# Kernel tuning notes

Hardware: AMD Instinct MI355X
Metric: run time of the kernel (lower is better)

Reference implementation:

```python
import jax, jax.numpy as jnp
import numpy as np

NL_IN = 0.5      # init kwarg nl_in
CONS = 1e-10     # epsilon added to rates
POISSON_GAIN = 20.0

def setup_inputs() -> dict:
    key = jax.random.key(0)
    k1, k2 = jax.random.split(key)
    shape = (8, 4, 28, 256, 256)  # (bs, c, s, h, w)
    spec_data = jax.random.uniform(k1, shape, dtype=jnp.float32)
    filt = jax.random.uniform(k2, shape, dtype=jnp.float32)
    return {"spec_data": spec_data, "filter": filt}

def reference(spec_data, filter):
    # cap_data = sum over (channel, spectral) dims -> [bs, h, w], then [bs, h, w, 1]
    cap = jnp.sum(spec_data * filter, axis=(1, 2))[..., None]

    # noise synthesis (need_noise=True path)
    poisson_t = jnp.full_like(cap, POISSON_GAIN * NL_IN)
    dark_t = jnp.full_like(cap, 1.0 * NL_IN)
    gauss_t = jnp.full_like(cap, 1.0 * NL_IN)
    peak = cap + CONS

    key = jax.random.key(1)
    kp, kd, kg = jax.random.split(key, 3)
    pnoisy = jax.random.poisson(kp, peak).astype(cap.dtype)
    dnoisy = jax.random.poisson(kd, dark_t).astype(cap.dtype)
    gnoisy = jax.random.normal(kg, cap.shape, dtype=cap.dtype) * gauss_t

    noisy = (pnoisy + dnoisy + gnoisy) * poisson_t / 255.0
    return (noisy, peak, dark_t, gauss_t ** 2)
```

## Files before the change

kernel.cpp:

```cpp
#include <hip/hip_runtime.h>
#include <cstdint>
#include <cstddef>

#pragma clang fp contract(off)

#define N_PIX    524288
#define CSPLANES 112
#define PLANE    65536
#define DCH      48
#define NBLK     256

struct TF2 { uint32_t a, b; };

__host__ __device__ constexpr uint32_t rotl32(uint32_t x, int d) {
  return (x << d) | (x >> (32 - d));
}

__host__ __device__ constexpr TF2 threefry(uint32_t k0, uint32_t k1,
                                           uint32_t c0, uint32_t c1) {
  uint32_t ks2 = k0 ^ k1 ^ 0x1BD11BDAu;
  uint32_t x0 = c0 + k0;
  uint32_t x1 = c1 + k1;
  const int R0[4] = {13, 15, 26, 6};
  const int R1[4] = {17, 29, 16, 24};
  for (int i = 0; i < 4; ++i) { x0 += x1; x1 = rotl32(x1, R0[i]); x1 ^= x0; }
  x0 += k1;  x1 += ks2 + 1u;
  for (int i = 0; i < 4; ++i) { x0 += x1; x1 = rotl32(x1, R1[i]); x1 ^= x0; }
  x0 += ks2; x1 += k0 + 2u;
  for (int i = 0; i < 4; ++i) { x0 += x1; x1 = rotl32(x1, R0[i]); x1 ^= x0; }
  x0 += k0;  x1 += k1 + 3u;
  for (int i = 0; i < 4; ++i) { x0 += x1; x1 = rotl32(x1, R1[i]); x1 ^= x0; }
  x0 += k1;  x1 += ks2 + 4u;
  for (int i = 0; i < 4; ++i) { x0 += x1; x1 = rotl32(x1, R0[i]); x1 ^= x0; }
  x0 += ks2; x1 += k0 + 5u;
  return TF2{x0, x1};
}

struct Chains {
  uint32_t kg0, kg1;
  uint32_t rj0a[DCH], rj0b[DCH], rj1a[DCH], rj1b[DCH];
  uint32_t kda[DCH], kdb[DCH];
  uint32_t kpa[DCH], kpb[DCH];
};

__host__ __device__ constexpr Chains make_chains() {
  Chains c{};
  TF2 kp = threefry(0u, 1u, 0u, 0u);
  TF2 kd = threefry(0u, 1u, 0u, 1u);
  TF2 kg = threefry(0u, 1u, 0u, 2u);
  c.kg0 = kg.a; c.kg1 = kg.b;
  {
    uint32_t a = kp.a, b = kp.b;
    for (int i = 0; i < DCH; ++i) {
      TF2 nk = threefry(a, b, 0u, 0u);
      TF2 s0 = threefry(a, b, 0u, 1u);
      TF2 s1 = threefry(a, b, 0u, 2u);
      c.rj0a[i] = s0.a; c.rj0b[i] = s0.b;
      c.rj1a[i] = s1.a; c.rj1b[i] = s1.b;
      a = nk.a; b = nk.b;
    }
  }
  {
    uint32_t a = kd.a, b = kd.b;
    for (int i = 0; i < DCH; ++i) {
      TF2 nk = threefry(a, b, 0u, 0u);
      TF2 sk = threefry(a, b, 0u, 1u);
      c.kda[i] = sk.a; c.kdb[i] = sk.b;
      a = nk.a; b = nk.b;
    }
  }
  {
    uint32_t a = kp.a, b = kp.b;
    for (int i = 0; i < DCH; ++i) {
      TF2 nk = threefry(a, b, 0u, 0u);
      TF2 sk = threefry(a, b, 0u, 1u);
      c.kpa[i] = sk.a; c.kpb[i] = sk.b;
      a = nk.a; b = nk.b;
    }
  }
  return c;
}

__constant__ Chains G = make_chains();

__device__ inline float u01(uint32_t k0, uint32_t k1, uint32_t j) {
  TF2 r = threefry(k0, k1, 0u, j);
  uint32_t bits = r.a ^ r.b;
  return __uint_as_float((bits >> 9) | 0x3F800000u) - 1.0f;
}

__device__ inline float xla_lgamma(float x_in) {
  float z = x_in - 1.0f;
  float x = 1.0f;
  x = x + 676.520368121885098567009190444019f    / ((z + 0.0f) + 1.0f);
  x = x + (-1259.13921672240287047156078755283f) / ((z + 1.0f) + 1.0f);
  x = x + 771.3234287776530788486528258894f      / ((z + 2.0f) + 1.0f);
  x = x + (-176.61502916214059906584551354f)     / ((z + 3.0f) + 1.0f);
  x = x + 12.507343278686904814458936853f        / ((z + 4.0f) + 1.0f);
  x = x + (-0.13857109526572011689554707f)       / ((z + 5.0f) + 1.0f);
  x = x + 9.984369578019570859563e-6f            / ((z + 6.0f) + 1.0f);
  x = x + 1.50563273514931155834e-7f             / ((z + 7.0f) + 1.0f);
  float t = 7.5f + z;
  float log_t = 2.0149030205422647f + log1pf(z / 7.5f);
  return 0.91893853320467274178f + ((z + 0.5f) - t / log_t) * log_t + logf(x);
}

__device__ inline float xla_erfinv(float xx) {
  float w = -log1pf(-(xx * xx));
  float p;
  if (w < 5.0f) {
    float ww = w - 2.5f;
    p = 2.81022636e-08f;
    p = 3.43273939e-07f + p * ww;
    p = -3.5233877e-06f + p * ww;
    p = -4.39150654e-06f + p * ww;
    p = 0.00021858087f + p * ww;
    p = -0.00125372503f + p * ww;
    p = -0.00417768164f + p * ww;
    p = 0.246640727f + p * ww;
    p = 1.50140941f + p * ww;
  } else {
    float ww = sqrtf(w) - 3.0f;
    p = -0.000200214257f;
    p = 0.000100950558f + p * ww;
    p = 0.00134934322f + p * ww;
    p = -0.00367342844f + p * ww;
    p = 0.00573950773f + p * ww;
    p = -0.0076224613f + p * ww;
    p = 0.00943887047f + p * ww;
    p = 1.00167406f + p * ww;
    p = 2.83297682f + p * ww;
  }
  return p * xx;
}

__device__ inline float xla_normal(uint32_t j) {
  const float lo = -0.999999940395355224609375f;
  float f = u01(G.kg0, G.kg1, j);
  float u = f * (1.0f - lo) + lo;
  u = fmaxf(lo, u);
  return 1.41421356237309504880f * xla_erfinv(u);
}

__device__ inline int knuth_sample(const uint32_t* ka, const uint32_t* kb,
                                   uint32_t j, float lam) {
  const float neg = -lam;
  int k = 0;
  float lp = 0.0f;
  #pragma unroll 1
  for (int i = 0; i < DCH; ++i) {
    if (!(lp > neg)) break;
    ++k;
    float uu = u01(ka[i], kb[i], j);
    lp = lp + logf(uu);
  }
  return k - 1;
}

struct RejC { float lam, loglam, a, b, inva, vr; };

__device__ inline RejC make_rc(float lam) {
  RejC rc;
  rc.lam = lam;
  rc.loglam = logf(lam);
  rc.b = 0.931f + 2.53f * sqrtf(lam);
  rc.a = -0.059f + 0.02483f * rc.b;
  rc.inva = 1.1239f + 1.1328f / (rc.b - 3.4f);
  rc.vr = 0.9277f - 3.6224f / (rc.b - 2.0f);
  return rc;
}

__device__ inline bool rej_step(const RejC& rc, uint32_t j, int i, float* kout) {
  float u = u01(G.rj0a[i], G.rj0b[i], j) - 0.5f;
  float v = u01(G.rj1a[i], G.rj1b[i], j);
  float us = 0.5f - fabsf(u);
  float k = floorf(((2.0f * rc.a / us + rc.b) * u + rc.lam) + 0.43f);
  *kout = k;
  bool accept1 = (us >= 0.07f) && (v <= rc.vr);
  if (accept1) return true;
  bool reject = (k < 0.0f) || ((us < 0.013f) && (v > us));
  if (reject) return false;
  float s = logf(v * rc.inva / (rc.a / (us * us) + rc.b));
  float t = (-rc.lam + k * rc.loglam) - xla_lgamma(k + 1.0f);
  return s <= t;
}

__device__ inline unsigned first_accept(const RejC& rc, uint32_t j) {
  unsigned F = DCH;
  #pragma unroll 1
  for (int i = 0; i < DCH; ++i) {
    float kc;
    if (rej_step(rc, j, i, &kc)) { F = (unsigned)(i + 1); break; }
  }
  return F;
}

__device__ inline float resolve_pix(const RejC& rc, float peak, uint32_t j, int T) {
  if (peak >= 10.0f) {
    float kk = -1.0f;
    #pragma unroll 1
    for (int i = T - 1; i >= 0; --i) {
      float kc;
      if (rej_step(rc, j, i, &kc)) { kk = kc; break; }
    }
    return (float)(int)kk;
  } else if (peak <= 0.0f) {
    return 0.0f;
  } else {
    return (float)knuth_sample(G.kpa, G.kpb, j, peak);
  }
}

__global__ __launch_bounds__(1024) void fused_kernel(const float* __restrict__ spec,
                                                     const float* __restrict__ filt,
                                                     float* __restrict__ out,
                                                     unsigned* __restrict__ sync) {
  const int tid = threadIdx.x;
  const int pixbase = blockIdx.x << 11;
  const int b_img = pixbase >> 16;
  const int hw = (pixbase & 65535) + (tid << 1);
  const size_t base = (size_t)b_img * ((size_t)CSPLANES * PLANE) + (size_t)hw;
  const float* sp = spec + base;
  const float* fp = filt + base;

  float a0 = 0.f, a1 = 0.f;
  #pragma unroll 8
  for (int cs = 0; cs < CSPLANES; ++cs) {
    const float2 s = *reinterpret_cast<const float2*>(sp + (size_t)cs * PLANE);
    const float2 f = *reinterpret_cast<const float2*>(fp + (size_t)cs * PLANE);
    a0 += s.x * f.x;
    a1 += s.y * f.y;
  }

  const uint32_t j0 = (uint32_t)(pixbase + (tid << 1));
  const uint32_t j1 = j0 + 1u;
  const float pk0 = a0 + 1e-10f;
  const float pk1 = a1 + 1e-10f;
  const float d0 = (float)knuth_sample(G.kda, G.kdb, j0, 0.5f);
  const float d1 = (float)knuth_sample(G.kda, G.kdb, j1, 0.5f);
  const float g0 = xla_normal(j0) * 0.5f;
  const float g1 = xla_normal(j1) * 0.5f;
  const RejC rc0 = make_rc(pk0);
  const RejC rc1 = make_rc(pk1);
  unsigned F0 = first_accept(rc0, j0);
  unsigned F1 = first_accept(rc1, j1);
  unsigned F = F0 > F1 ? F0 : F1;

  for (int off = 32; off; off >>= 1) {
    unsigned o = (unsigned)__shfl_down((int)F, off, 64);
    F = F > o ? F : o;
  }
  __shared__ unsigned sred[16];
  __shared__ int sT;
  if ((tid & 63) == 0) sred[tid >> 6] = F;
  __syncthreads();
  if (tid == 0) {
    unsigned m = sred[0];
    #pragma unroll
    for (int i = 1; i < 16; ++i) m = m > sred[i] ? m : sred[i];
    __hip_atomic_fetch_max(&sync[0], m, __ATOMIC_RELAXED, __HIP_MEMORY_SCOPE_AGENT);
    __hip_atomic_fetch_add(&sync[1], 1u, __ATOMIC_ACQ_REL, __HIP_MEMORY_SCOPE_AGENT);
    while (__hip_atomic_load(&sync[1], __ATOMIC_ACQUIRE, __HIP_MEMORY_SCOPE_AGENT) < (unsigned)NBLK) {
      __builtin_amdgcn_s_sleep(8);
    }
    sT = (int)__hip_atomic_load(&sync[0], __ATOMIC_RELAXED, __HIP_MEMORY_SCOPE_AGENT);
  }
  __syncthreads();
  const int T = sT;

  const float pv0 = resolve_pix(rc0, pk0, j0, T);
  const float pv1 = resolve_pix(rc1, pk1, j1, T);
  const float n0 = ((pv0 + d0) + g0) * 10.0f / 255.0f;
  const float n1 = ((pv1 + d1) + g1) * 10.0f / 255.0f;

  *reinterpret_cast<float2*>(out + j0)             = make_float2(n0, n1);
  *reinterpret_cast<float2*>(out + N_PIX + j0)     = make_float2(pk0, pk1);
  *reinterpret_cast<float2*>(out + 2 * N_PIX + j0) = make_float2(0.5f, 0.5f);
  *reinterpret_cast<float2*>(out + 3 * N_PIX + j0) = make_float2(0.25f, 0.25f);
}

extern "C" void kernel_launch(void* const* d_in, const int* in_sizes, int n_in,
                              void* d_out, int out_size, void* d_ws, size_t ws_size,
                              hipStream_t stream) {
  (void)in_sizes; (void)n_in; (void)out_size; (void)ws_size;
  const float* spec = (const float*)d_in[0];
  const float* filt = (const float*)d_in[1];
  float* out = (float*)d_out;
  unsigned* sync = (unsigned*)d_ws;
  (void)hipMemsetAsync(d_ws, 0, 2 * sizeof(unsigned), stream);
  hipLaunchKernelGGL(fused_kernel, dim3(NBLK), dim3(1024), 0, stream,
                     spec, filt, out, sync);
}
```

Baseline: 498.1 us.

## Use one pixel per thread with 512 blocks and batched plane loads

Each thread now handles one pixel instead of two, so the grid doubles to 512 blocks of 1024 threads. The reduction loop issues 16 independent scalar loads of spec and filter before accumulating, raising memory-level parallelism. Launch bounds now request higher occupancy. In exchange, loads narrow from float2 to scalar, and the grid-wide spin barrier must wait on twice as many blocks, which must all be co-resident to avoid deadlock.

```diff
diff --git a/kernel.cpp b/kernel.cpp
--- a/kernel.cpp
+++ b/kernel.cpp
@@ -8,7 +8,7 @@
 #define CSPLANES 112
 #define PLANE    65536
 #define DCH      48
-#define NBLK     256
+#define NBLK     512
 
 struct TF2 { uint32_t a, b; };
 
@@ -211,40 +211,36 @@
   }
 }
 
-__global__ __launch_bounds__(1024) void fused_kernel(const float* __restrict__ spec,
-                                                     const float* __restrict__ filt,
-                                                     float* __restrict__ out,
-                                                     unsigned* __restrict__ sync) {
+__global__ __launch_bounds__(1024, 8) void fused_kernel(const float* __restrict__ spec,
+                                                        const float* __restrict__ filt,
+                                                        float* __restrict__ out,
+                                                        unsigned* __restrict__ sync) {
   const int tid = threadIdx.x;
-  const int pixbase = blockIdx.x << 11;
+  const int pixbase = blockIdx.x << 10;
   const int b_img = pixbase >> 16;
-  const int hw = (pixbase & 65535) + (tid << 1);
+  const int hw = (pixbase & 65535) + tid;
   const size_t base = (size_t)b_img * ((size_t)CSPLANES * PLANE) + (size_t)hw;
   const float* sp = spec + base;
   const float* fp = filt + base;
 
-  float a0 = 0.f, a1 = 0.f;
-  #pragma unroll 8
-  for (int cs = 0; cs < CSPLANES; ++cs) {
-    const float2 s = *reinterpret_cast<const float2*>(sp + (size_t)cs * PLANE);
-    const float2 f = *reinterpret_cast<const float2*>(fp + (size_t)cs * PLANE);
-    a0 += s.x * f.x;
-    a1 += s.y * f.y;
-  }
-
-  const uint32_t j0 = (uint32_t)(pixbase + (tid << 1));
-  const uint32_t j1 = j0 + 1u;
-  const float pk0 = a0 + 1e-10f;
-  const float pk1 = a1 + 1e-10f;
-  const float d0 = (float)knuth_sample(G.kda, G.kdb, j0, 0.5f);
-  const float d1 = (float)knuth_sample(G.kda, G.kdb, j1, 0.5f);
-  const float g0 = xla_normal(j0) * 0.5f;
-  const float g1 = xla_normal(j1) * 0.5f;
-  const RejC rc0 = make_rc(pk0);
-  const RejC rc1 = make_rc(pk1);
-  unsigned F0 = first_accept(rc0, j0);
-  unsigned F1 = first_accept(rc1, j1);
-  unsigned F = F0 > F1 ? F0 : F1;
+  float a = 0.f;
+  #pragma unroll 1
+  for (int c = 0; c < CSPLANES; c += 16) {
+    float ss[16], ff[16];
+    #pragma unroll
+    for (int i = 0; i < 16; ++i) ss[i] = sp[(size_t)(c + i) * PLANE];
+    #pragma unroll
+    for (int i = 0; i < 16; ++i) ff[i] = fp[(size_t)(c + i) * PLANE];
+    #pragma unroll
+    for (int i = 0; i < 16; ++i) a = a + ss[i] * ff[i];
+  }
+
+  const uint32_t j = (uint32_t)(pixbase + tid);
+  const float pk = a + 1e-10f;
+  const float d = (float)knuth_sample(G.kda, G.kdb, j, 0.5f);
+  const float g = xla_normal(j) * 0.5f;
+  const RejC rc = make_rc(pk);
+  unsigned F = first_accept(rc, j);
 
   for (int off = 32; off; off >>= 1) {
     unsigned o = (unsigned)__shfl_down((int)F, off, 64);
@@ -268,15 +264,13 @@
   __syncthreads();
   const int T = sT;
 
-  const float pv0 = resolve_pix(rc0, pk0, j0, T);
-  const float pv1 = resolve_pix(rc1, pk1, j1, T);
-  const float n0 = ((pv0 + d0) + g0) * 10.0f / 255.0f;
-  const float n1 = ((pv1 + d1) + g1) * 10.0f / 255.0f;
-
-  *reinterpret_cast<float2*>(out + j0)             = make_float2(n0, n1);
-  *reinterpret_cast<float2*>(out + N_PIX + j0)     = make_float2(pk0, pk1);
-  *reinterpret_cast<float2*>(out + 2 * N_PIX + j0) = make_float2(0.5f, 0.5f);
-  *reinterpret_cast<float2*>(out + 3 * N_PIX + j0) = make_float2(0.25f, 0.25f);
+  const float pv = resolve_pix(rc, pk, j, T);
+  const float n = ((pv + d) + g) * 10.0f / 255.0f;
+
+  out[j]             = n;
+  out[N_PIX + j]     = pk;
+  out[2 * N_PIX + j] = 0.5f;
+  out[3 * N_PIX + j] = 0.25f;
 }
 
 extern "C" void kernel_launch(void* const* d_in, const int* in_sizes, int n_in,
```

Result: slower. 542.6 us (+8.9%).
